# Kernel tuning notes

Hardware: AMD Instinct MI355X
Metric: run time of the kernel (lower is better)

## Reference

```python
import jax, jax.numpy as jnp
import numpy as np

N_NODES = 2048
N_EDGES = 49152
R_MAX = 6.0
NUM_BASIS = 8
N_LAYERS = 4
AVG_NEIGH = 24.0
MUL_S, MUL_V = 32, 16                 # hidden irreps = 32x0e + 16x1o
N_SC_OUT = MUL_S + MUL_V              # 48 scalar channels before gate (32 scalars + 16 gates)
HID = MUL_S + 3 * MUL_V               # 80 = hidden feature dim
RAD_H = 64
# tp path weight sizes: (0e x 0e -> 0e), (1o x 1o -> 0e), (0e x 1o -> 1o), (1o x 0e -> 1o), (1o x 2e -> 1o)
N1 = MUL_S * N_SC_OUT; N2 = MUL_V * N_SC_OUT; N3 = MUL_S * MUL_V; N4 = MUL_V * MUL_V; N5 = MUL_V * MUL_V
WNUM = N1 + N2 + N3 + N4 + N5         # 3328

# orthonormal symmetric-traceless basis for real l=2 (order: xy, yz, z2, xz, x2-y2)
_s2 = 1.0 / np.sqrt(2.0); _s6 = 1.0 / np.sqrt(6.0)
_Q = np.zeros((5, 3, 3), np.float32)
_Q[0, 0, 1] = _Q[0, 1, 0] = _s2
_Q[1, 1, 2] = _Q[1, 2, 1] = _s2
_Q[2, 0, 0] = _Q[2, 1, 1] = -_s6; _Q[2, 2, 2] = 2 * _s6
_Q[3, 0, 2] = _Q[3, 2, 0] = _s2
_Q[4, 0, 0] = _s2; _Q[4, 1, 1] = -_s2
Q2 = jnp.asarray(_Q)


def _sph(d):
    # component-normalized real spherical harmonics of unit vectors d [E,3]
    x, y, z = d[:, 0], d[:, 1], d[:, 2]
    y1 = jnp.sqrt(3.0) * d
    c = jnp.sqrt(15.0)
    y2 = jnp.stack([c * x * y, c * y * z, 0.5 * jnp.sqrt(5.0) * (3 * z * z - 1.0),
                    c * x * z, 0.5 * c * (x * x - y * y)], -1)
    return y1, y2


def _bessel_cutoff(r):
    # Bessel radial basis * polynomial cutoff (p=6); r [E,1]
    n = jnp.arange(1, NUM_BASIS + 1, dtype=jnp.float32)
    rbf = jnp.sqrt(2.0 / R_MAX) * jnp.sin(n * jnp.pi * r / R_MAX) / r
    u = r / R_MAX
    f = (1.0 - 28.0 * u ** 6 + 48.0 * u ** 7 - 21.0 * u ** 8) * (u < 1.0)
    return rbf * f


def _lin(h, Ws, Wv):
    # e3nn Linear hidden -> hidden (per-irrep channel mixing, fan-in normalized)
    s = h[:, :MUL_S] @ Ws / jnp.sqrt(float(MUL_S))
    v = jnp.einsum('nui,uw->nwi', h[:, MUL_S:].reshape(-1, MUL_V, 3), Wv) / jnp.sqrt(float(MUL_V))
    return jnp.concatenate([s, v.reshape(-1, 3 * MUL_V)], -1)


def reference(x, pos, edge_index, embed_w, proj_w, lin_ws, lin_wv, sc_ws, sc_wv,
              mlp_w1, mlp_b1, mlp_w2, mlp_b2, mlp_w3, mlp_b3):
    src, dst = edge_index[0], edge_index[1]
    rel = pos[dst] - pos[src]                                   # pos_i - pos_j
    r = jnp.maximum(jnp.linalg.norm(rel, axis=-1, keepdims=True), 1e-6)
    d = rel / r
    y1, y2 = _sph(d)
    rbf = _bessel_cutoff(r)                                     # [E, 8]
    # embed: only 0e->0e path exists; 1o part starts at zero
    h = jnp.concatenate([x @ embed_w / jnp.sqrt(16.0),
                         jnp.zeros((x.shape[0], 3 * MUL_V), x.dtype)], -1)
    for l in range(N_LAYERS):
        x_res = h
        x_self = _lin(h, sc_ws[l], sc_wv[l])
        hx = _lin(h, lin_ws[l], lin_wv[l])
        # radial MLP -> per-edge tensor-product weights
        f = jax.nn.silu(rbf @ mlp_w1[l] + mlp_b1[l])
        f = jax.nn.silu(f @ mlp_w2[l] + mlp_b2[l])
        w = f @ mlp_w3[l] + mlp_b3[l]                           # [E, WNUM]
        o = 0
        w1 = w[:, o:o + N1].reshape(-1, MUL_S, N_SC_OUT); o += N1
        w2 = w[:, o:o + N2].reshape(-1, MUL_V, N_SC_OUT); o += N2
        w3 = w[:, o:o + N3].reshape(-1, MUL_S, MUL_V);    o += N3
        w4 = w[:, o:o + N4].reshape(-1, MUL_V, MUL_V);    o += N4
        w5 = w[:, o:o + N5].reshape(-1, MUL_V, MUL_V)
        s_j = hx[src, :MUL_S]
        v_j = hx[src, MUL_S:].reshape(-1, MUL_V, 3)
        # scalar outputs: (0e x 0e -> 0e) and (1o x 1o -> 0e)
        p2 = jnp.einsum('eui,ei->eu', v_j, y1) / jnp.sqrt(3.0)
        out_s = (jnp.einsum('eu,euw->ew', s_j, w1) + jnp.einsum('eu,euw->ew', p2, w2)) / jnp.sqrt(48.0)
        # vector outputs: (0e x 1o -> 1o), (1o x 0e -> 1o), (1o x 2e -> 1o)
        q3 = jnp.einsum('eu,ei->eui', s_j, y1)
        q5 = jnp.sqrt(3.0 / 5.0) * jnp.einsum('eui,em,mij->euj', v_j, y2, Q2)
        out_v = (jnp.einsum('eui,euw->ewi', q3, w3) + jnp.einsum('eui,euw->ewi', v_j, w4)
                 + jnp.einsum('eui,euw->ewi', q5, w5)) / jnp.sqrt(64.0)
        msg = jnp.concatenate([out_s, out_v.reshape(-1, 3 * MUL_V)], -1)   # [E, 96]
        agg = jax.ops.segment_sum(msg, dst, num_segments=N_NODES) / jnp.sqrt(AVG_NEIGH)
        # Gate: silu on scalars, sigmoid gates scale 1o channels
        sc = jax.nn.silu(agg[:, :MUL_S])
        g = jax.nn.sigmoid(agg[:, MUL_S:MUL_S + MUL_V])
        vec = agg[:, MUL_S + MUL_V:].reshape(-1, MUL_V, 3) * g[:, :, None]
        h = x_res + x_self + jnp.concatenate([sc, vec.reshape(-1, 3 * MUL_V)], -1)
    return h[:, :MUL_S] @ proj_w / jnp.sqrt(float(MUL_S))


def setup_inputs() -> dict:
    key = jax.random.key(0)
    ks = jax.random.split(key, 16)
    nrm = jax.random.normal
    return {
        'x': nrm(ks[0], (N_NODES, 16), jnp.float32),
        'pos': 2.0 * nrm(ks[1], (N_NODES, 3), jnp.float32),
        'edge_index': jax.random.randint(ks[2], (2, N_EDGES), 0, N_NODES),
        'embed_w': nrm(ks[3], (16, MUL_S), jnp.float32),
        'proj_w': nrm(ks[4], (MUL_S, 32), jnp.float32),
        'lin_ws': nrm(ks[5], (N_LAYERS, MUL_S, MUL_S), jnp.float32),
        'lin_wv': nrm(ks[6], (N_LAYERS, MUL_V, MUL_V), jnp.float32),
        'sc_ws': nrm(ks[7], (N_LAYERS, MUL_S, MUL_S), jnp.float32),
        'sc_wv': nrm(ks[8], (N_LAYERS, MUL_V, MUL_V), jnp.float32),
        'mlp_w1': nrm(ks[9], (N_LAYERS, NUM_BASIS, RAD_H), jnp.float32) / np.sqrt(NUM_BASIS),
        'mlp_b1': jnp.zeros((N_LAYERS, RAD_H), jnp.float32),
        'mlp_w2': nrm(ks[10], (N_LAYERS, RAD_H, RAD_H), jnp.float32) / np.sqrt(RAD_H),
        'mlp_b2': jnp.zeros((N_LAYERS, RAD_H), jnp.float32),
        'mlp_w3': nrm(ks[11], (N_LAYERS, RAD_H, WNUM), jnp.float32) / np.sqrt(RAD_H),
        'mlp_b3': jnp.zeros((N_LAYERS, WNUM), jnp.float32),
    }
```

## Files before the change

### kernel.cpp

```cpp
#include <hip/hip_runtime.h>
#include <math.h>

#define NN 2048
#define NE 49152
#define WNUM 3328

typedef __attribute__((ext_vector_type(8))) _Float16 half8;
typedef __attribute__((ext_vector_type(4))) float f32x4;

__device__ __forceinline__ float silu_f(float x){ return x / (1.0f + expf(-x)); }
__device__ __forceinline__ float sigm_f(float x){ return 1.0f / (1.0f + expf(-x)); }

__global__ void geom_kernel(const float* __restrict__ pos, const int* __restrict__ ei,
                            float* __restrict__ egeo, int* __restrict__ cnt) {
  int e = blockIdx.x * 256 + threadIdx.x;
  if (e >= NE) return;
  int s = ei[e], d = ei[NE + e];
  atomicAdd(&cnt[d], 1);
  float rx = pos[d*3+0] - pos[s*3+0];
  float ry = pos[d*3+1] - pos[s*3+1];
  float rz = pos[d*3+2] - pos[s*3+2];
  float r = sqrtf(rx*rx + ry*ry + rz*rz);
  r = fmaxf(r, 1e-6f);
  float x = rx / r, y = ry / r, z = rz / r;
  const float s3 = 1.7320508075688772f;
  const float c15 = 3.872983346207417f;
  float y2_0 = c15 * x * y;
  float y2_1 = c15 * y * z;
  float y2_2 = 1.118033988749895f * (3.0f*z*z - 1.0f);
  float y2_3 = c15 * x * z;
  float y2_4 = 1.9364916731037085f * (x*x - y*y);
  const float q2 = 0.7071067811865476f;
  const float q6 = 0.4082482904638631f;
  float* g = egeo + (size_t)e * 20;
  g[0] = s3 * x; g[1] = s3 * y; g[2] = s3 * z;
  g[3+0] = -q6*y2_2 + q2*y2_4;
  g[3+1] =  q2*y2_0;
  g[3+2] =  q2*y2_3;
  g[3+3] =  q2*y2_0;
  g[3+4] = -q6*y2_2 - q2*y2_4;
  g[3+5] =  q2*y2_1;
  g[3+6] =  q2*y2_3;
  g[3+7] =  q2*y2_1;
  g[3+8] =  2.0f*q6*y2_2;
  float u = r / 6.0f;
  float fc = 0.0f;
  if (u < 1.0f) {
    float u2=u*u, u3=u2*u, u6=u3*u3, u7=u6*u, u8=u7*u;
    fc = 1.0f - 28.0f*u6 + 48.0f*u7 - 21.0f*u8;
  }
  const float pref = 0.5773502691896258f;
  const float pi6 = 0.5235987755982988f;
  #pragma unroll
  for (int n = 1; n <= 8; n++) {
    g[12 + n - 1] = pref * sinf((float)n * pi6 * r) / r * fc;
  }
}

__global__ void scan_kernel(const int* __restrict__ cnt, int* __restrict__ offs,
                            int* __restrict__ cursor) {
  __shared__ int part[256];
  int t = threadIdx.x;
  int local[8];
  int s = 0;
  #pragma unroll
  for (int j = 0; j < 8; j++) { local[j] = s; s += cnt[t*8 + j]; }
  part[t] = s;
  __syncthreads();
  for (int off = 1; off < 256; off <<= 1) {
    int v = part[t];
    int add = (t >= off) ? part[t - off] : 0;
    __syncthreads();
    part[t] = v + add;
    __syncthreads();
  }
  int excl = (t == 0) ? 0 : part[t-1];
  #pragma unroll
  for (int j = 0; j < 8; j++) {
    int o = excl + local[j];
    offs[t*8 + j] = o;
    cursor[t*8 + j] = o;
  }
  if (t == 255) offs[2048] = part[255];
}

__global__ void scatter_kernel(const int* __restrict__ ei, int* __restrict__ cursor,
                               int* __restrict__ eidx) {
  int e = blockIdx.x * 256 + threadIdx.x;
  if (e >= NE) return;
  int d = ei[NE + e];
  int p = atomicAdd(&cursor[d], 1);
  eidx[p] = e;
}

__global__ void conv_w3_kernel(const float* __restrict__ w3g, _Float16* __restrict__ w3h) {
  int tid = blockIdx.x * 256 + threadIdx.x;
  if (tid >= 16 * WNUM) return;
  int n = tid % WNUM;
  int lq = tid / WNUM;
  int quad = lq & 3, l = lq >> 2;
  const float* src = w3g + (size_t)l * 64 * WNUM + n;
  int idx = n >> 4, L = n & 15;
  _Float16* dst = w3h + ((size_t)(l * 208 + idx) * 2) * 512 + (quad*16 + L) * 8;
  half8 h0, h1;
  #pragma unroll
  for (int j = 0; j < 8; j++) {
    h0[j] = (_Float16)src[(size_t)(quad*8 + j) * WNUM];
    h1[j] = (_Float16)src[(size_t)(32 + quad*8 + j) * WNUM];
  }
  *(half8*)(dst)       = h0;
  *(half8*)(dst + 512) = h1;
}

__global__ void embed_kernel(const float* __restrict__ x, const float* __restrict__ ew,
                             float* __restrict__ h) {
  int idx = blockIdx.x * 256 + threadIdx.x;
  if (idx >= NN * 80) return;
  int n = idx / 80, c = idx % 80;
  float v = 0.0f;
  if (c < 32) {
    #pragma unroll
    for (int j = 0; j < 16; j++) v += x[n*16 + j] * ew[j*32 + c];
    v *= 0.25f;
  }
  h[idx] = v;
}

#define NB_R (NE/16)
#define NB_N ((NN*160 + 255)/256)
__global__ void rn_fused_kernel(const float* __restrict__ egeo,
                                const float* __restrict__ w1, const float* __restrict__ b1,
                                const float* __restrict__ w2, const float* __restrict__ b2,
                                _Float16* __restrict__ f_h,
                                const float* __restrict__ h,
                                const float* __restrict__ lws, const float* __restrict__ lwv,
                                const float* __restrict__ sws, const float* __restrict__ swv,
                                float* __restrict__ hx, float* __restrict__ xself, int l) {
  __shared__ float h1s[16][64];
  if (blockIdx.x < NB_R) {
    int ty = threadIdx.x >> 6, dk = threadIdx.x & 63;
    int e0b = blockIdx.x * 16 + ty * 4;
    const float* w1l = w1 + (size_t)l * 8 * 64;
    const float* w2l = w2 + (size_t)l * 64 * 64;
    float b1v = b1[l*64 + dk];
    #pragma unroll
    for (int k = 0; k < 4; ++k) {
      const float* rb = egeo + (size_t)(e0b + k) * 20 + 12;
      float acc = b1v;
      #pragma unroll
      for (int j = 0; j < 8; j++) acc += rb[j] * w1l[j*64 + dk];
      h1s[ty*4 + k][dk] = silu_f(acc);
    }
    __syncthreads();
    float b2v = b2[l*64 + dk];
    float o0 = b2v, o1 = b2v, o2 = b2v, o3 = b2v;
    #pragma unroll 8
    for (int j = 0; j < 64; ++j) {
      float w = w2l[j*64 + dk];
      o0 += h1s[ty*4+0][j] * w;
      o1 += h1s[ty*4+1][j] * w;
      o2 += h1s[ty*4+2][j] * w;
      o3 += h1s[ty*4+3][j] * w;
    }
    f_h[(size_t)(e0b+0)*64 + dk] = (_Float16)silu_f(o0);
    f_h[(size_t)(e0b+1)*64 + dk] = (_Float16)silu_f(o1);
    f_h[(size_t)(e0b+2)*64 + dk] = (_Float16)silu_f(o2);
    f_h[(size_t)(e0b+3)*64 + dk] = (_Float16)silu_f(o3);
  } else {
    int idx = (blockIdx.x - NB_R) * 256 + threadIdx.x;
    if (idx >= NN * 160) return;
    int which = (idx >= NN * 80) ? 1 : 0;
    int r = which ? idx - NN*80 : idx;
    int n = r / 80, c = r % 80;
    const float* Ws = (which ? sws : lws) + (size_t)l * 1024;
    const float* Wv = (which ? swv : lwv) + (size_t)l * 256;
    float v = 0.0f;
    if (c < 32) {
      #pragma unroll 8
      for (int u = 0; u < 32; u++) v += h[n*80 + u] * Ws[u*32 + c];
      v *= 0.17677669529663687f;
    } else {
      int oc = c - 32, wch = oc / 3, i = oc % 3;
      #pragma unroll
      for (int u = 0; u < 16; u++) v += h[n*80 + 32 + u*3 + i] * Wv[u*16 + wch];
      v *= 0.25f;
    }
    (which ? xself : hx)[n*80 + c] = v;
  }
}

__launch_bounds__(256, 2)
__global__ void edge_msg_kernel(const int* __restrict__ ei, const float* __restrict__ egeo,
                                const _Float16* __restrict__ f_h,
                                const float* __restrict__ hx,
                                const _Float16* __restrict__ w3h,
                                const float* __restrict__ b3g,
                                float* __restrict__ msg, int l) {
  __shared__ float smem[15616];
  float* sT    = smem;
  float* p2T   = smem + 2048;
  float* q3T   = smem + 3072;
  float* vT    = smem + 6144;
  float* q5T   = smem + 9216;
  float* biasL = smem + 12288;
  float* poolA = smem;
  float* poolB = smem + 3072;
  float* poolC = smem + 6144;

  const int t = threadIdx.x;
  const int e0 = blockIdx.x * 64;
  const float* b3l = b3g + (size_t)l * WNUM;

  for (int i = t; i < WNUM; i += 256) biasL[i] = b3l[i];
  for (int idx = t; idx < 64*80; idx += 256) {
    int e = idx / 80, c = idx % 80;
    int src = ei[e0 + e];
    float val = hx[(size_t)src*80 + c];
    if (c < 32) sT[c*64 + e] = val; else vT[(c-32)*64 + e] = val;
  }
  __syncthreads();
  for (int idx = t; idx < 64*16; idx += 256) {
    int u = idx >> 6, e = idx & 63;
    const float* g = &egeo[(size_t)(e0+e)*20];
    float a = vT[(u*3)*64+e]*g[0] + vT[(u*3+1)*64+e]*g[1] + vT[(u*3+2)*64+e]*g[2];
    p2T[u*64 + e] = a * 0.5773502691896258f;
  }
  for (int idx = t; idx < 64*48; idx += 256) {
    int o = idx >> 6, e = idx & 63;
    int u = o / 3, jj = o % 3;
    const float* g = &egeo[(size_t)(e0+e)*20];
    q3T[o*64 + e] = sT[u*64 + e] * g[jj];
    float a = vT[(u*3)*64+e]*g[3+jj] + vT[(u*3+1)*64+e]*g[6+jj] + vT[(u*3+2)*64+e]*g[9+jj];
    q5T[o*64 + e] = a * 0.7745966692414834f;
  }

  const int wv = t >> 6, lane = t & 63, L = lane & 15, quad = lane >> 4;
  const int qb = quad * 4;

  half8 Ah[4][2];
  #pragma unroll
  for (int g = 0; g < 4; ++g) {
    const half8* fA = (const half8*)(f_h + (size_t)(e0 + g*16 + L)*64);
    Ah[g][0] = fA[quad];
    Ah[g][1] = fA[4 + quad];
  }
  __syncthreads();

  const _Float16* wb = w3h + (size_t)l * 208 * 1024 + lane * 8;
  half8 pb0[4], pb1[4];
  float bs[4];

#define PRIME(START)                                                          \
  { _Pragma("unroll")                                                         \
    for (int _s = 0; _s < 4; ++_s) {                                          \
      const _Float16* _wn = wb + (size_t)((START) + _s) * 1024;               \
      pb0[_s] = *(const half8*)_wn;                                           \
      pb1[_s] = *(const half8*)(_wn + 512);                                   \
      bs[_s] = biasL[((START) + _s)*16 + L];                                  \
    } }

#define GCORE(IDX, CO, OKCOND)                                                \
  f32x4 a0, a1, a2, a3;                                                       \
  { half8 _B0 = pb0[(CO)&3], _B1 = pb1[(CO)&3];                               \
    float _bb = bs[(CO)&3];                                                   \
    if (OKCOND) {                                                             \
      const _Float16* _wn = wb + (size_t)((IDX) + 4) * 1024;                  \
      pb0[(CO)&3] = *(const half8*)_wn;                                       \
      pb1[(CO)&3] = *(const half8*)(_wn + 512);                               \
      bs[(CO)&3] = biasL[((IDX) + 4)*16 + L];                                 \
    }                                                                         \
    a0 = (f32x4){_bb,_bb,_bb,_bb}; a1 = a0; a2 = a0; a3 = a0;                 \
    a0 = __builtin_amdgcn_mfma_f32_16x16x32_f16(Ah[0][0], _B0, a0, 0,0,0);    \
    a0 = __builtin_amdgcn_mfma_f32_16x16x32_f16(Ah[0][1], _B1, a0, 0,0,0);    \
    a1 = __builtin_amdgcn_mfma_f32_16x16x32_f16(Ah[1][0], _B0, a1, 0,0,0);    \
    a1 = __builtin_amdgcn_mfma_f32_16x16x32_f16(Ah[1][1], _B1, a1, 0,0,0);    \
    a2 = __builtin_amdgcn_mfma_f32_16x16x32_f16(Ah[2][0], _B0, a2, 0,0,0);    \
    a2 = __builtin_amdgcn_mfma_f32_16x16x32_f16(Ah[2][1], _B1, a2, 0,0,0);    \
    a3 = __builtin_amdgcn_mfma_f32_16x16x32_f16(Ah[3][0], _B0, a3, 0,0,0);    \
    a3 = __builtin_amdgcn_mfma_f32_16x16x32_f16(Ah[3][1], _B1, a3, 0,0,0);    \
  }

  const float S48 = 0.14433756729740645f;
  const float S64 = 0.125f;

  if (wv <= 1) {
    f32x4 ms[4][3];
    #pragma unroll
    for (int g = 0; g < 4; ++g)
      #pragma unroll
      for (int j = 0; j < 3; ++j) ms[g][j] = (f32x4){0,0,0,0};
    const int ustart = wv * 16, istart = wv * 48, iend = istart + 48;
    PRIME(istart);
    for (int u4 = 0; u4 < 16; u4 += 4) {
      #pragma unroll
      for (int uu = 0; uu < 4; ++uu) {
        const int u = u4 + uu;
        f32x4 f0 = *(const f32x4*)&sT[(ustart+u)*64 + qb];
        f32x4 f1 = *(const f32x4*)&sT[(ustart+u)*64 + 16 + qb];
        f32x4 f2 = *(const f32x4*)&sT[(ustart+u)*64 + 32 + qb];
        f32x4 f3 = *(const f32x4*)&sT[(ustart+u)*64 + 48 + qb];
        #pragma unroll
        for (int j = 0; j < 3; ++j) {
          const int CO = uu*3 + j;
          const int idx = istart + u4*3 + CO;
          GCORE(idx, CO, idx + 4 < iend);
          ms[0][j] += f0*a0; ms[1][j] += f1*a1; ms[2][j] += f2*a2; ms[3][j] += f3*a3;
        }
      }
    }
    float* pool = (wv == 0) ? poolA : poolB;
    __syncthreads();
    #pragma unroll
    for (int g = 0; g < 4; ++g)
      #pragma unroll
      for (int j = 0; j < 3; ++j)
        #pragma unroll
        for (int r = 0; r < 4; ++r)
          pool[(g*16 + qb + r)*48 + j*16 + L] = ms[g][j][r];
    __syncthreads();
  } else if (wv == 2) {
    f32x4 ms[4][3], mv[4][3];
    #pragma unroll
    for (int g = 0; g < 4; ++g)
      #pragma unroll
      for (int j = 0; j < 3; ++j) { ms[g][j] = (f32x4){0,0,0,0}; mv[g][j] = (f32x4){0,0,0,0}; }
    PRIME(96);
    for (int u4 = 0; u4 < 16; u4 += 4) {
      #pragma unroll
      for (int uu = 0; uu < 4; ++uu) {
        const int u = u4 + uu;
        f32x4 f0 = *(const f32x4*)&p2T[u*64 + qb];
        f32x4 f1 = *(const f32x4*)&p2T[u*64 + 16 + qb];
        f32x4 f2 = *(const f32x4*)&p2T[u*64 + 32 + qb];
        f32x4 f3 = *(const f32x4*)&p2T[u*64 + 48 + qb];
        #pragma unroll
        for (int j = 0; j < 3; ++j) {
          const int CO = uu*3 + j;
          const int idx = 96 + u4*3 + CO;
          GCORE(idx, CO, idx + 4 < 144);
          ms[0][j] += f0*a0; ms[1][j] += f1*a1; ms[2][j] += f2*a2; ms[3][j] += f3*a3;
        }
      }
    }
    PRIME(176);
    for (int u4 = 0; u4 < 16; u4 += 4) {
      #pragma unroll
      for (int uu = 0; uu < 4; ++uu) {
        const int u = u4 + uu;
        const int idx = 176 + u;
        GCORE(idx, uu, idx + 4 < 192);
        #pragma unroll
        for (int i = 0; i < 3; ++i) {
          mv[0][i] += *(const f32x4*)&vT[(u*3+i)*64 + qb]      * a0;
          mv[1][i] += *(const f32x4*)&vT[(u*3+i)*64 + 16 + qb] * a1;
          mv[2][i] += *(const f32x4*)&vT[(u*3+i)*64 + 32 + qb] * a2;
          mv[3][i] += *(const f32x4*)&vT[(u*3+i)*64 + 48 + qb] * a3;
        }
      }
    }
    __syncthreads();
    #pragma unroll
    for (int g = 0; g < 4; ++g)
      #pragma unroll
      for (int i = 0; i < 3; ++i)
        #pragma unroll
        for (int r = 0; r < 4; ++r)
          poolC[(g*16 + qb + r)*48 + i*16 + L] = mv[g][i][r];
    __syncthreads();
    #pragma unroll
    for (int g = 0; g < 4; ++g) {
      #pragma unroll
      for (int r = 0; r < 4; ++r) {
        const int eb = g*16 + qb + r;
        float* mp = msg + (size_t)(e0 + eb)*96;
        #pragma unroll
        for (int j = 0; j < 3; ++j)
          mp[j*16 + L] = (ms[g][j][r] + poolA[eb*48 + j*16 + L] + poolB[eb*48 + j*16 + L]) * S48;
      }
    }
  } else {
    f32x4 mv[4][3];
    #pragma unroll
    for (int g = 0; g < 4; ++g)
      #pragma unroll
      for (int i = 0; i < 3; ++i) mv[g][i] = (f32x4){0,0,0,0};
    PRIME(144);
    for (int u4 = 0; u4 < 32; u4 += 4) {
      #pragma unroll
      for (int uu = 0; uu < 4; ++uu) {
        const int u = u4 + uu;
        const int idx = 144 + u;
        GCORE(idx, uu, idx + 4 < 176);
        #pragma unroll
        for (int i = 0; i < 3; ++i) {
          mv[0][i] += *(const f32x4*)&q3T[(u*3+i)*64 + qb]      * a0;
          mv[1][i] += *(const f32x4*)&q3T[(u*3+i)*64 + 16 + qb] * a1;
          mv[2][i] += *(const f32x4*)&q3T[(u*3+i)*64 + 32 + qb] * a2;
          mv[3][i] += *(const f32x4*)&q3T[(u*3+i)*64 + 48 + qb] * a3;
        }
      }
    }
    PRIME(192);
    for (int u4 = 0; u4 < 16; u4 += 4) {
      #pragma unroll
      for (int uu = 0; uu < 4; ++uu) {
        const int u = u4 + uu;
        const int idx = 192 + u;
        GCORE(idx, uu, idx + 4 < 208);
        #pragma unroll
        for (int i = 0; i < 3; ++i) {
          mv[0][i] += *(const f32x4*)&q5T[(u*3+i)*64 + qb]      * a0;
          mv[1][i] += *(const f32x4*)&q5T[(u*3+i)*64 + 16 + qb] * a1;
          mv[2][i] += *(const f32x4*)&q5T[(u*3+i)*64 + 32 + qb] * a2;
          mv[3][i] += *(const f32x4*)&q5T[(u*3+i)*64 + 48 + qb] * a3;
        }
      }
    }
    __syncthreads();
    __syncthreads();
    #pragma unroll
    for (int g = 0; g < 4; ++g) {
      #pragma unroll
      for (int r = 0; r < 4; ++r) {
        const int eb = g*16 + qb + r;
        float* mp = msg + (size_t)(e0 + eb)*96;
        #pragma unroll
        for (int i = 0; i < 3; ++i)
          mp[48 + 3*L + i] = (mv[g][i][r] + poolC[eb*48 + i*16 + L]) * S64;
      }
    }
  }
#undef GCORE
#undef PRIME
}

__global__ void agg_update_kernel(const float* __restrict__ msg, const int* __restrict__ offs,
                                  const int* __restrict__ eidx,
                                  const float* __restrict__ xself, float* __restrict__ h) {
  __shared__ float sagg[2][96];
  int t = threadIdx.x;
  int half = t >> 7, tt = t & 127;
  int n = blockIdx.x * 2 + half;
  if (tt < 96) {
    int b = offs[n], e = offs[n+1];
    float acc = 0.0f, acc2 = 0.0f;
    int j = b;
    for (; j + 1 < e; j += 2) {
      acc  += msg[(size_t)eidx[j]*96 + tt];
      acc2 += msg[(size_t)eidx[j+1]*96 + tt];
    }
    if (j < e) acc += msg[(size_t)eidx[j]*96 + tt];
    sagg[half][tt] = (acc + acc2) * 0.20412414523193154f;
  }
  __syncthreads();
  if (tt < 80) {
    float a;
    if (tt < 32) {
      a = silu_f(sagg[half][tt]);
    } else {
      int oc = tt - 32, wch = oc / 3;
      a = sagg[half][48 + oc] * sigm_f(sagg[half][32 + wch]);
    }
    h[(size_t)n*80 + tt] = h[(size_t)n*80 + tt] + xself[(size_t)n*80 + tt] + a;
  }
}

__global__ void proj_kernel(const float* __restrict__ h, const float* __restrict__ pw,
                            float* __restrict__ out) {
  int idx = blockIdx.x * 256 + threadIdx.x;
  if (idx >= NN * 32) return;
  int n = idx / 32, c = idx % 32;
  float acc = 0.0f;
  #pragma unroll 8
  for (int u = 0; u < 32; u++) acc += h[n*80 + u] * pw[u*32 + c];
  out[idx] = acc * 0.17677669529663687f;
}

extern "C" void kernel_launch(void* const* d_in, const int* in_sizes, int n_in,
                              void* d_out, int out_size, void* d_ws, size_t ws_size,
                              hipStream_t stream) {
  const float* x       = (const float*)d_in[0];
  const float* pos     = (const float*)d_in[1];
  const int*   ei      = (const int*)  d_in[2];
  const float* embed_w = (const float*)d_in[3];
  const float* proj_w  = (const float*)d_in[4];
  const float* lin_ws  = (const float*)d_in[5];
  const float* lin_wv  = (const float*)d_in[6];
  const float* sc_ws   = (const float*)d_in[7];
  const float* sc_wv   = (const float*)d_in[8];
  const float* mlp_w1  = (const float*)d_in[9];
  const float* mlp_b1  = (const float*)d_in[10];
  const float* mlp_w2  = (const float*)d_in[11];
  const float* mlp_b2  = (const float*)d_in[12];
  const float* mlp_w3  = (const float*)d_in[13];
  const float* mlp_b3  = (const float*)d_in[14];
  float* out = (float*)d_out;

  float* ws    = (float*)d_ws;
  float* egeo  = ws;
  float* h     = egeo  + (size_t)NE*20;
  float* hx    = h     + (size_t)NN*80;
  float* xself = hx    + (size_t)NN*80;
  float* msg   = xself + (size_t)NN*80;
  _Float16* f_h = (_Float16*)(msg + (size_t)NE*96);
  _Float16* w3h = f_h + (size_t)NE*64;
  int* cnt    = (int*)(w3h + (size_t)4*208*1024);
  int* offs   = cnt + NN;
  int* cursor = offs + NN + 1;
  int* eidxb  = cursor + NN;

  hipMemsetAsync(cnt, 0, NN*sizeof(int), stream);
  geom_kernel<<<(NE + 255)/256, 256, 0, stream>>>(pos, ei, egeo, cnt);
  scan_kernel<<<1, 256, 0, stream>>>(cnt, offs, cursor);
  scatter_kernel<<<NE/256, 256, 0, stream>>>(ei, cursor, eidxb);
  conv_w3_kernel<<<(16*WNUM + 255)/256, 256, 0, stream>>>(mlp_w3, w3h);
  embed_kernel<<<(NN*80 + 255)/256, 256, 0, stream>>>(x, embed_w, h);

  for (int l = 0; l < 4; l++) {
    rn_fused_kernel<<<NB_R + NB_N, 256, 0, stream>>>(egeo, mlp_w1, mlp_b1, mlp_w2, mlp_b2,
                                                     f_h, h, lin_ws, lin_wv, sc_ws, sc_wv,
                                                     hx, xself, l);
    edge_msg_kernel<<<NE/64, 256, 0, stream>>>(ei, egeo, f_h, hx, w3h, mlp_b3, msg, l);
    agg_update_kernel<<<NN/2, 256, 0, stream>>>(msg, offs, eidxb, xself, h);
  }
  proj_kernel<<<(NN*32 + 255)/256, 256, 0, stream>>>(h, proj_w, out);
}
```

Measured before the change: 478.5 us.

## Batch radial MLP across layers and fuse aggregation with next-layer linears

The radial MLP for all four layers is now computed once up front into a per-layer f_h buffer. The embedding is fused with the first layer's self and linear projections. Each aggregation kernel also computes the next layer's hx/xself, or the final projection on the last layer, which drops separate per-layer launches and extra reads of h. In edge_msg, the bias is read from global memory instead of being staged in LDS, so shared memory shrinks and launch bounds rise to 3 blocks per CU, at some risk of register pressure or spills.

```diff
diff --git a/kernel.cpp b/kernel.cpp
--- a/kernel.cpp
+++ b/kernel.cpp
@@ -112,97 +112,92 @@
   *(half8*)(dst + 512) = h1;
 }
 
-__global__ void embed_kernel(const float* __restrict__ x, const float* __restrict__ ew,
-                             float* __restrict__ h) {
-  int idx = blockIdx.x * 256 + threadIdx.x;
-  if (idx >= NN * 80) return;
-  int n = idx / 80, c = idx % 80;
+#define NBR1 (NE/16)
+__global__ void radial_all_kernel(const float* __restrict__ egeo,
+                                  const float* __restrict__ w1, const float* __restrict__ b1,
+                                  const float* __restrict__ w2, const float* __restrict__ b2,
+                                  _Float16* __restrict__ f_h) {
+  __shared__ float h1s[16][64];
+  int l = blockIdx.x / NBR1;
+  int bb = blockIdx.x % NBR1;
+  int ty = threadIdx.x >> 6, dk = threadIdx.x & 63;
+  int e0b = bb * 16 + ty * 4;
+  const float* w1l = w1 + (size_t)l * 8 * 64;
+  const float* w2l = w2 + (size_t)l * 64 * 64;
+  _Float16* fl = f_h + (size_t)l * NE * 64;
+  float b1v = b1[l*64 + dk];
+  #pragma unroll
+  for (int k = 0; k < 4; ++k) {
+    const float* rb = egeo + (size_t)(e0b + k) * 20 + 12;
+    float acc = b1v;
+    #pragma unroll
+    for (int j = 0; j < 8; j++) acc += rb[j] * w1l[j*64 + dk];
+    h1s[ty*4 + k][dk] = silu_f(acc);
+  }
+  __syncthreads();
+  float b2v = b2[l*64 + dk];
+  float o0 = b2v, o1 = b2v, o2 = b2v, o3 = b2v;
+  #pragma unroll 8
+  for (int j = 0; j < 64; ++j) {
+    float w = w2l[j*64 + dk];
+    o0 += h1s[ty*4+0][j] * w;
+    o1 += h1s[ty*4+1][j] * w;
+    o2 += h1s[ty*4+2][j] * w;
+    o3 += h1s[ty*4+3][j] * w;
+  }
+  fl[(size_t)(e0b+0)*64 + dk] = (_Float16)silu_f(o0);
+  fl[(size_t)(e0b+1)*64 + dk] = (_Float16)silu_f(o1);
+  fl[(size_t)(e0b+2)*64 + dk] = (_Float16)silu_f(o2);
+  fl[(size_t)(e0b+3)*64 + dk] = (_Float16)silu_f(o3);
+}
+
+__global__ void embed_prep_kernel(const float* __restrict__ x, const float* __restrict__ ew,
+                                  const float* __restrict__ lws0, const float* __restrict__ sws0,
+                                  float* __restrict__ h, float* __restrict__ hx,
+                                  float* __restrict__ xself) {
+  __shared__ float hs[8][32];
+  int t = threadIdx.x;
+  int nl = t >> 5, c = t & 31;
+  int n = blockIdx.x * 8 + nl;
   float v = 0.0f;
-  if (c < 32) {
-    #pragma unroll
-    for (int j = 0; j < 16; j++) v += x[n*16 + j] * ew[j*32 + c];
-    v *= 0.25f;
-  }
-  h[idx] = v;
-}
-
-#define NB_R (NE/16)
-#define NB_N ((NN*160 + 255)/256)
-__global__ void rn_fused_kernel(const float* __restrict__ egeo,
-                                const float* __restrict__ w1, const float* __restrict__ b1,
-                                const float* __restrict__ w2, const float* __restrict__ b2,
-                                _Float16* __restrict__ f_h,
-                                const float* __restrict__ h,
-                                const float* __restrict__ lws, const float* __restrict__ lwv,
-                                const float* __restrict__ sws, const float* __restrict__ swv,
-                                float* __restrict__ hx, float* __restrict__ xself, int l) {
-  __shared__ float h1s[16][64];
-  if (blockIdx.x < NB_R) {
-    int ty = threadIdx.x >> 6, dk = threadIdx.x & 63;
-    int e0b = blockIdx.x * 16 + ty * 4;
-    const float* w1l = w1 + (size_t)l * 8 * 64;
-    const float* w2l = w2 + (size_t)l * 64 * 64;
-    float b1v = b1[l*64 + dk];
-    #pragma unroll
-    for (int k = 0; k < 4; ++k) {
-      const float* rb = egeo + (size_t)(e0b + k) * 20 + 12;
-      float acc = b1v;
-      #pragma unroll
-      for (int j = 0; j < 8; j++) acc += rb[j] * w1l[j*64 + dk];
-      h1s[ty*4 + k][dk] = silu_f(acc);
-    }
-    __syncthreads();
-    float b2v = b2[l*64 + dk];
-    float o0 = b2v, o1 = b2v, o2 = b2v, o3 = b2v;
-    #pragma unroll 8
-    for (int j = 0; j < 64; ++j) {
-      float w = w2l[j*64 + dk];
-      o0 += h1s[ty*4+0][j] * w;
-      o1 += h1s[ty*4+1][j] * w;
-      o2 += h1s[ty*4+2][j] * w;
-      o3 += h1s[ty*4+3][j] * w;
-    }
-    f_h[(size_t)(e0b+0)*64 + dk] = (_Float16)silu_f(o0);
-    f_h[(size_t)(e0b+1)*64 + dk] = (_Float16)silu_f(o1);
-    f_h[(size_t)(e0b+2)*64 + dk] = (_Float16)silu_f(o2);
-    f_h[(size_t)(e0b+3)*64 + dk] = (_Float16)silu_f(o3);
-  } else {
-    int idx = (blockIdx.x - NB_R) * 256 + threadIdx.x;
-    if (idx >= NN * 160) return;
-    int which = (idx >= NN * 80) ? 1 : 0;
-    int r = which ? idx - NN*80 : idx;
-    int n = r / 80, c = r % 80;
-    const float* Ws = (which ? sws : lws) + (size_t)l * 1024;
-    const float* Wv = (which ? swv : lwv) + (size_t)l * 256;
-    float v = 0.0f;
-    if (c < 32) {
+  #pragma unroll
+  for (int j = 0; j < 16; j++) v += x[n*16 + j] * ew[j*32 + c];
+  v *= 0.25f;
+  hs[nl][c] = v;
+  h[(size_t)n*80 + c] = v;
+  for (int idx = t; idx < 8*48; idx += 256) {
+    int nn = blockIdx.x * 8 + idx / 48;
+    h[(size_t)nn*80 + 32 + idx % 48] = 0.0f;
+  }
+  __syncthreads();
+  for (int idx = t; idx < 2*8*80; idx += 256) {
+    int which = idx / 640, r = idx % 640;
+    int nl2 = r / 80, cc = r % 80;
+    int n2 = blockIdx.x * 8 + nl2;
+    float o = 0.0f;
+    if (cc < 32) {
+      const float* W = which ? sws0 : lws0;
       #pragma unroll 8
-      for (int u = 0; u < 32; u++) v += h[n*80 + u] * Ws[u*32 + c];
-      v *= 0.17677669529663687f;
-    } else {
-      int oc = c - 32, wch = oc / 3, i = oc % 3;
-      #pragma unroll
-      for (int u = 0; u < 16; u++) v += h[n*80 + 32 + u*3 + i] * Wv[u*16 + wch];
-      v *= 0.25f;
-    }
-    (which ? xself : hx)[n*80 + c] = v;
-  }
-}
-
-__launch_bounds__(256, 2)
+      for (int u = 0; u < 32; u++) o += hs[nl2][u] * W[u*32 + cc];
+      o *= 0.17677669529663687f;
+    }
+    (which ? xself : hx)[(size_t)n2*80 + cc] = o;
+  }
+}
+
+__launch_bounds__(256, 3)
 __global__ void edge_msg_kernel(const int* __restrict__ ei, const float* __restrict__ egeo,
                                 const _Float16* __restrict__ f_h,
                                 const float* __restrict__ hx,
                                 const _Float16* __restrict__ w3h,
                                 const float* __restrict__ b3g,
                                 float* __restrict__ msg, int l) {
-  __shared__ float smem[15616];
+  __shared__ float smem[12288];
   float* sT    = smem;
   float* p2T   = smem + 2048;
   float* q3T   = smem + 3072;
   float* vT    = smem + 6144;
   float* q5T   = smem + 9216;
-  float* biasL = smem + 12288;
   float* poolA = smem;
   float* poolB = smem + 3072;
   float* poolC = smem + 6144;
@@ -211,7 +206,6 @@
   const int e0 = blockIdx.x * 64;
   const float* b3l = b3g + (size_t)l * WNUM;
 
-  for (int i = t; i < WNUM; i += 256) biasL[i] = b3l[i];
   for (int idx = t; idx < 64*80; idx += 256) {
     int e = idx / 80, c = idx % 80;
     int src = ei[e0 + e];
@@ -256,7 +250,7 @@
       const _Float16* _wn = wb + (size_t)((START) + _s) * 1024;               \
       pb0[_s] = *(const half8*)_wn;                                           \
       pb1[_s] = *(const half8*)(_wn + 512);                                   \
-      bs[_s] = biasL[((START) + _s)*16 + L];                                  \
+      bs[_s] = b3l[((START) + _s)*16 + L];                                    \
     } }
 
 #define GCORE(IDX, CO, OKCOND)                                                \
@@ -267,7 +261,7 @@
       const _Float16* _wn = wb + (size_t)((IDX) + 4) * 1024;                  \
       pb0[(CO)&3] = *(const half8*)_wn;                                       \
       pb1[(CO)&3] = *(const half8*)(_wn + 512);                               \
-      bs[(CO)&3] = biasL[((IDX) + 4)*16 + L];                                 \
+      bs[(CO)&3] = b3l[((IDX) + 4)*16 + L];                                   \
     }                                                                         \
     a0 = (f32x4){_bb,_bb,_bb,_bb}; a1 = a0; a2 = a0; a3 = a0;                 \
     a0 = __builtin_amdgcn_mfma_f32_16x16x32_f16(Ah[0][0], _B0, a0, 0,0,0);    \
@@ -434,46 +428,77 @@
 #undef PRIME
 }
 
-__global__ void agg_update_kernel(const float* __restrict__ msg, const int* __restrict__ offs,
-                                  const int* __restrict__ eidx,
-                                  const float* __restrict__ xself, float* __restrict__ h) {
-  __shared__ float sagg[2][96];
+__global__ void agg_fused_kernel(const float* __restrict__ msg, const int* __restrict__ offs,
+                                 const int* __restrict__ eidx,
+                                 const float* __restrict__ xself_in, float* __restrict__ h,
+                                 const float* __restrict__ lwsN, const float* __restrict__ lwvN,
+                                 const float* __restrict__ swsN, const float* __restrict__ swvN,
+                                 float* __restrict__ hx_out, float* __restrict__ xself_out,
+                                 const float* __restrict__ pw, float* __restrict__ out,
+                                 int last) {
+  __shared__ float sagg[4][96];
+  __shared__ float hnew[4][80];
   int t = threadIdx.x;
-  int half = t >> 7, tt = t & 127;
-  int n = blockIdx.x * 2 + half;
-  if (tt < 96) {
+  int nb = blockIdx.x * 4;
+  for (int idx = t; idx < 4*96; idx += 256) {
+    int nl = idx / 96, c = idx % 96;
+    int n = nb + nl;
     int b = offs[n], e = offs[n+1];
     float acc = 0.0f, acc2 = 0.0f;
     int j = b;
     for (; j + 1 < e; j += 2) {
-      acc  += msg[(size_t)eidx[j]*96 + tt];
-      acc2 += msg[(size_t)eidx[j+1]*96 + tt];
-    }
-    if (j < e) acc += msg[(size_t)eidx[j]*96 + tt];
-    sagg[half][tt] = (acc + acc2) * 0.20412414523193154f;
-  }
-  __syncthreads();
-  if (tt < 80) {
+      acc  += msg[(size_t)eidx[j]*96 + c];
+      acc2 += msg[(size_t)eidx[j+1]*96 + c];
+    }
+    if (j < e) acc += msg[(size_t)eidx[j]*96 + c];
+    sagg[nl][c] = (acc + acc2) * 0.20412414523193154f;
+  }
+  __syncthreads();
+  for (int idx = t; idx < 4*80; idx += 256) {
+    int nl = idx / 80, c = idx % 80;
+    int n = nb + nl;
     float a;
-    if (tt < 32) {
-      a = silu_f(sagg[half][tt]);
+    if (c < 32) {
+      a = silu_f(sagg[nl][c]);
     } else {
-      int oc = tt - 32, wch = oc / 3;
-      a = sagg[half][48 + oc] * sigm_f(sagg[half][32 + wch]);
-    }
-    h[(size_t)n*80 + tt] = h[(size_t)n*80 + tt] + xself[(size_t)n*80 + tt] + a;
-  }
-}
-
-__global__ void proj_kernel(const float* __restrict__ h, const float* __restrict__ pw,
-                            float* __restrict__ out) {
-  int idx = blockIdx.x * 256 + threadIdx.x;
-  if (idx >= NN * 32) return;
-  int n = idx / 32, c = idx % 32;
-  float acc = 0.0f;
-  #pragma unroll 8
-  for (int u = 0; u < 32; u++) acc += h[n*80 + u] * pw[u*32 + c];
-  out[idx] = acc * 0.17677669529663687f;
+      int oc = c - 32, wch = oc / 3;
+      a = sagg[nl][48 + oc] * sigm_f(sagg[nl][32 + wch]);
+    }
+    float hn = h[(size_t)n*80 + c] + xself_in[(size_t)n*80 + c] + a;
+    hnew[nl][c] = hn;
+    h[(size_t)n*80 + c] = hn;
+  }
+  __syncthreads();
+  if (!last) {
+    for (int idx = t; idx < 2*4*80; idx += 256) {
+      int which = idx / 320, r = idx % 320;
+      int nl = r / 80, c = r % 80;
+      int n = nb + nl;
+      const float* Ws = which ? swsN : lwsN;
+      const float* Wv = which ? swvN : lwvN;
+      float v = 0.0f;
+      if (c < 32) {
+        #pragma unroll 8
+        for (int u = 0; u < 32; u++) v += hnew[nl][u] * Ws[u*32 + c];
+        v *= 0.17677669529663687f;
+      } else {
+        int oc = c - 32, wch = oc / 3, i = oc % 3;
+        #pragma unroll
+        for (int u = 0; u < 16; u++) v += hnew[nl][32 + u*3 + i] * Wv[u*16 + wch];
+        v *= 0.25f;
+      }
+      (which ? xself_out : hx_out)[(size_t)n*80 + c] = v;
+    }
+  } else {
+    for (int idx = t; idx < 4*32; idx += 256) {
+      int nl = idx / 32, c = idx % 32;
+      int n = nb + nl;
+      float acc = 0.0f;
+      #pragma unroll 8
+      for (int u = 0; u < 32; u++) acc += hnew[nl][u] * pw[u*32 + c];
+      out[(size_t)n*32 + c] = acc * 0.17677669529663687f;
+    }
+  }
 }
 
 extern "C" void kernel_launch(void* const* d_in, const int* in_sizes, int n_in,
@@ -503,7 +528,7 @@
   float* xself = hx    + (size_t)NN*80;
   float* msg   = xself + (size_t)NN*80;
   _Float16* f_h = (_Float16*)(msg + (size_t)NE*96);
-  _Float16* w3h = f_h + (size_t)NE*64;
+  _Float16* w3h = f_h + (size_t)4*NE*64;
   int* cnt    = (int*)(w3h + (size_t)4*208*1024);
   int* offs   = cnt + NN;
   int* cursor = offs + NN + 1;
@@ -514,14 +539,19 @@
   scan_kernel<<<1, 256, 0, stream>>>(cnt, offs, cursor);
   scatter_kernel<<<NE/256, 256, 0, stream>>>(ei, cursor, eidxb);
   conv_w3_kernel<<<(16*WNUM + 255)/256, 256, 0, stream>>>(mlp_w3, w3h);
-  embed_kernel<<<(NN*80 + 255)/256, 256, 0, stream>>>(x, embed_w, h);
+  radial_all_kernel<<<NBR1*4, 256, 0, stream>>>(egeo, mlp_w1, mlp_b1, mlp_w2, mlp_b2, f_h);
+  embed_prep_kernel<<<NN/8, 256, 0, stream>>>(x, embed_w, lin_ws, sc_ws, h, hx, xself);
 
   for (int l = 0; l < 4; l++) {
-    rn_fused_kernel<<<NB_R + NB_N, 256, 0, stream>>>(egeo, mlp_w1, mlp_b1, mlp_w2, mlp_b2,
-                                                     f_h, h, lin_ws, lin_wv, sc_ws, sc_wv,
-                                                     hx, xself, l);
-    edge_msg_kernel<<<NE/64, 256, 0, stream>>>(ei, egeo, f_h, hx, w3h, mlp_b3, msg, l);
-    agg_update_kernel<<<NN/2, 256, 0, stream>>>(msg, offs, eidxb, xself, h);
-  }
-  proj_kernel<<<(NN*32 + 255)/256, 256, 0, stream>>>(h, proj_w, out);
-}
+    edge_msg_kernel<<<NE/64, 256, 0, stream>>>(ei, egeo, f_h + (size_t)l*NE*64, hx,
+                                               w3h, mlp_b3, msg, l);
+    int last = (l == 3);
+    agg_fused_kernel<<<NN/4, 256, 0, stream>>>(
+        msg, offs, eidxb, xself, h,
+        lin_ws + (size_t)(l+1 < 4 ? l+1 : 0) * 1024,
+        lin_wv + (size_t)(l+1 < 4 ? l+1 : 0) * 256,
+        sc_ws  + (size_t)(l+1 < 4 ? l+1 : 0) * 1024,
+        sc_wv  + (size_t)(l+1 < 4 ? l+1 : 0) * 256,
+        hx, xself, proj_w, out, last);
+  }
+}
```

Measured after the change: 600.4 us. 25.5% more time.
